# Optimization experiments

Hardware: AMD Instinct MI355X
Metric: run time of the kernel (lower is better)

Reference implementation:

```python
import jax, jax.numpy as jnp
import numpy as np

E = 65536            # total entities (flattened batch*history*slots)
ENTITY_SIZE = 256
NUM_SPECIES, NUM_ABILITIES, NUM_ITEMS, NUM_ACTIONS = 512, 128, 256, 512
# feature layout (column index in entity row)
SPECIES, ABILITY, ITEM = 0, 1, 2
SCALAR_FEATS = list(range(3, 16))   # level..fainted
SCALAR_MAX = [101, 2, 2, 32, 3, 8, 16, 2, 2, 2, 8, 4, 2]
BOOST_FEATS = list(range(16, 23))   # 7 boosts
BOOST_MAX = 13
VOL0, VOL8 = 23, 31                 # 9 uint16 volatile words
TC0, TC1 = 32, 33                   # 2 uint16 typechange words
MOVE0 = 34                          # 4 move-id tokens
NUM_FEATS = 38
HP_RATIO = 6
CONCAT_DIM = 512 + 128 + 256 + sum(SCALAR_MAX) + 7 * BOOST_MAX + 9 * 16 + 2 * 16 + 1  # = 1348

MAXES = np.ones(NUM_FEATS, dtype=np.int32)
MAXES[SPECIES], MAXES[ABILITY], MAXES[ITEM] = NUM_SPECIES, NUM_ABILITIES, NUM_ITEMS
for f, m in zip(SCALAR_FEATS, SCALAR_MAX):
    MAXES[f] = m
for f in BOOST_FEATS:
    MAXES[f] = BOOST_MAX
MAXES[VOL0:VOL8 + 1] = 65536
MAXES[TC0:TC1 + 1] = 65536
MAXES[MOVE0:MOVE0 + 4] = NUM_ACTIONS


def bits16(x):
    # x int32 [..., k] -> float bits [..., k*16]
    b = (x[..., None] >> jnp.arange(16, dtype=jnp.int32)) & 1
    return b.astype(jnp.float32).reshape(*x.shape[:-1], -1)


def setup_inputs() -> dict:
    key = jax.random.key(0)
    ks = jax.random.split(key, 12)
    u = jax.random.uniform(ks[0], (E, NUM_FEATS))
    entity = (u * jnp.asarray(MAXES, dtype=jnp.float32)).astype(jnp.int32)
    s = 0.02
    return {
        'entity': entity,
        'species_tbl': jax.random.normal(ks[1], (NUM_SPECIES, 512), jnp.float32) * s,
        'ability_tbl': jax.random.normal(ks[2], (NUM_ABILITIES, 128), jnp.float32) * s,
        'item_tbl': jax.random.normal(ks[3], (NUM_ITEMS, 256), jnp.float32) * s,
        'species_emb': jax.random.normal(ks[4], (NUM_SPECIES, ENTITY_SIZE), jnp.float32) * s,
        'ability_emb': jax.random.normal(ks[5], (NUM_ABILITIES, ENTITY_SIZE), jnp.float32) * s,
        'item_emb': jax.random.normal(ks[6], (NUM_ITEMS, ENTITY_SIZE), jnp.float32) * s,
        'actions_emb': jax.random.normal(ks[7], (NUM_ACTIONS, ENTITY_SIZE), jnp.float32) * s,
        'agg_w': jax.random.normal(ks[8], (CONCAT_DIM, ENTITY_SIZE), jnp.float32) * s,
        'agg_b': jnp.zeros((ENTITY_SIZE,), jnp.float32),
        'mlp_w': jax.random.normal(ks[9], (ENTITY_SIZE, ENTITY_SIZE), jnp.float32) * s,
        'mlp_b': jnp.zeros((ENTITY_SIZE,), jnp.float32),
    }


def reference(entity, species_tbl, ability_tbl, item_tbl, species_emb, ability_emb,
              item_emb, actions_emb, agg_w, agg_b, mlp_w, mlp_b):
    sp, ab, it = entity[:, SPECIES], entity[:, ABILITY], entity[:, ITEM]
    # pretrained one-hot / feature-table gathers
    enc = [species_tbl[sp], ability_tbl[ab], item_tbl[it]]
    # small scalar one-hots
    enc += [jax.nn.one_hot(entity[:, f], m, dtype=jnp.float32)
            for f, m in zip(SCALAR_FEATS, SCALAR_MAX)]
    # boost one-hots
    enc += [jax.nn.one_hot(entity[:, f], BOOST_MAX, dtype=jnp.float32) for f in BOOST_FEATS]
    # hex/binary encodings of volatile + typechange words
    enc.append(bits16(entity[:, VOL0:VOL8 + 1]))       # [E,144]
    enc.append(bits16(entity[:, TC0:TC1 + 1]))         # [E,32]
    # continuous feature (hp ratio)
    enc.append((entity[:, HP_RATIO].astype(jnp.float32) / 31.0)[:, None])
    concat = jnp.concatenate(enc, axis=-1)             # [E,1348]
    emb_sum = (species_emb[sp] + ability_emb[ab] + item_emb[it]
               + actions_emb[entity[:, MOVE0]] + actions_emb[entity[:, MOVE0 + 1]]
               + actions_emb[entity[:, MOVE0 + 2]] + actions_emb[entity[:, MOVE0 + 3]])
    x = concat @ agg_w + agg_b + emb_sum               # SumEmbeddings
    x = jax.nn.relu(x) @ mlp_w + mlp_b                 # MLP((entity_size,))
    mask = jnp.logical_and(sp != 0, sp != 1)           # not NULL / not PAD
    return jnp.where(mask[:, None], x, 0.0)
```

## Files before the change

kernel.cpp:

```cpp
#include <hip/hip_runtime.h>

#define NFEAT 38

typedef __attribute__((ext_vector_type(8))) short bf16x8;
typedef __attribute__((ext_vector_type(4))) float f32x4;
typedef __attribute__((ext_vector_type(2))) float f32x2;
typedef __attribute__((ext_vector_type(4))) unsigned int u32x4;

#define R_SP   0
#define R_AB   512
#define R_IT   640
#define R_T1   896
#define R_T2   1300
#define R_T3   1428
#define R_T4   1452
#define R_T5   1484
#define R_T6   1548
#define R_T7   1717
#define R_T8   1886
#define R_T9   2055
#define R_ACT  2068
#define NROWS  2580

#define B_FUSED  0
#define B_WMLP   224
#define B_WBITS  288
#define B_MERGED 336
#define B_IDXS   757
#define NB_PREP  821

__device__ __forceinline__ unsigned short f2bf(float f) {
    unsigned int u = __float_as_uint(f);
    u += 0x7fffu + ((u >> 16) & 1u);
    return (unsigned short)(u >> 16);
}

__global__ __launch_bounds__(1024) void k_prep(
    const float* __restrict__ sp_tbl, const float* __restrict__ ab_tbl,
    const float* __restrict__ it_tbl, const float* __restrict__ sp_emb,
    const float* __restrict__ ab_emb, const float* __restrict__ it_emb,
    const float* __restrict__ act_emb, const float* __restrict__ agg_w,
    const float* __restrict__ agg_b,  const float* __restrict__ mlp_w,
    const int* __restrict__ ent,
    unsigned short* __restrict__ tbl, unsigned short* __restrict__ wfrag,
    unsigned short* __restrict__ wbits, unsigned int* __restrict__ ridx)
{
    __shared__ float rowbuf[4 * 512];
    __shared__ float part[4][4][256];
    int blk = blockIdx.x, t = threadIdx.x, c = t & 255;
#define W(x) agg_w[(size_t)(x) * 256 + c]

    if (blk < B_WMLP) {
        int r0 = blk << 2;
        const float* src; const float* emb; int len, wbase; bool add_b;
        if (r0 < 512)      { src = sp_tbl + (size_t)r0 * 512;           emb = sp_emb + (size_t)r0 * 256;           len = 512; wbase = 0;   add_b = true;  }
        else if (r0 < 640) { int q = r0 - 512; src = ab_tbl + (size_t)q * 128; emb = ab_emb + (size_t)q * 256; len = 128; wbase = 512; add_b = false; }
        else               { int q = r0 - 640; src = it_tbl + (size_t)q * 256; emb = it_emb + (size_t)q * 256; len = 256; wbase = 640; add_b = false; }
        int tot = len << 2;
        for (int i = t; i < tot; i += 1024) rowbuf[i] = src[i];
        __syncthreads();
        int kq   = t >> 8;
        int len4 = len >> 2;
        int kbeg = kq * len4, kend = kbeg + len4;
        float a0 = 0.f, a1 = 0.f, a2 = 0.f, a3 = 0.f;
        #pragma unroll 4
        for (int k = kbeg; k < kend; ++k) {
            float w = W(wbase + k);
            a0 += rowbuf[k] * w;
            a1 += rowbuf[len + k] * w;
            a2 += rowbuf[2 * len + k] * w;
            a3 += rowbuf[3 * len + k] * w;
        }
        part[0][kq][c] = a0; part[1][kq][c] = a1;
        part[2][kq][c] = a2; part[3][kq][c] = a3;
        __syncthreads();
        int row = t >> 8;
        float s = part[row][0][c] + part[row][1][c] + part[row][2][c] + part[row][3][c]
                + emb[row * 256 + c] + (add_b ? agg_b[c] : 0.f);
        tbl[(size_t)(r0 + row) * 256 + c] = f2bf(s);
        return;
    }
    if (blk < B_WBITS) {
        int idx = ((blk - B_WMLP) << 10) + t;
        int j   = idx & 7;
        int fl  = (idx >> 3) & 63;
        int k0g = (idx >> 9) & 7;
        int nt  = idx >> 12;
        int k   = k0g * 32 + (fl >> 4) * 8 + j;
        int col = nt * 16 + (fl & 15);
        wfrag[idx] = f2bf(mlp_w[(size_t)k * 256 + col]);
        return;
    }
    if (blk < B_MERGED) {
        int idx = ((blk - B_WBITS) << 10) + t;
        int j   = idx & 7;
        int ln  = (idx >> 3) & 63;
        int r2  = idx >> 9;
        int kt  = r2 % 6;
        int nt  = r2 / 6;
        int k   = kt * 32 + ((ln >> 4) << 3) + j;
        int col = (nt << 4) + (ln & 15);
        float v = (k < 176) ? agg_w[(size_t)(1171 + k) * 256 + col] : 0.f;
        wbits[idx] = f2bf(v);
        return;
    }
    if (blk < B_IDXS) {
        int r = ((blk - B_MERGED) << 2) + (t >> 8);
        int row; float acc;
        if (r < 404)       { int f3 = r >> 2, f4 = (r >> 1) & 1, f5 = r & 1;
                             acc = W(896 + f3) + W(997 + f4) + W(999 + f5); row = R_T1 + r; }
        else if (r < 532)  { int i = r - 404; int f6 = i >> 2, f11 = (i >> 1) & 1, f12 = i & 1;
                             acc = W(1001 + f6) + (float)f6 * (1.f / 31.f) * W(1347)
                                 + W(1062 + f11) + W(1064 + f12); row = R_T2 + i; }
        else if (r < 556)  { int i = r - 532; acc = W(1033 + (i >> 3)) + W(1036 + (i & 7)); row = R_T3 + i; }
        else if (r < 588)  { int i = r - 556; acc = W(1044 + (i >> 1)) + W(1060 + (i & 1)); row = R_T4 + i; }
        else if (r < 652)  { int i = r - 588; acc = W(1066 + (i >> 3)) + W(1074 + ((i >> 1) & 3)) + W(1078 + (i & 1)); row = R_T5 + i; }
        else if (r < 821)  { int i = r - 652; acc = W(1080 + i / 13) + W(1093 + i % 13); row = R_T6 + i; }
        else if (r < 990)  { int i = r - 821; acc = W(1106 + i / 13) + W(1119 + i % 13); row = R_T7 + i; }
        else if (r < 1159) { int i = r - 990; acc = W(1132 + i / 13) + W(1145 + i % 13); row = R_T8 + i; }
        else if (r < 1172) { int i = r - 1159; acc = W(1158 + i); row = R_T9 + i; }
        else               { int i = r - 1172; acc = act_emb[(size_t)i * 256 + c]; row = R_ACT + i; }
        tbl[(size_t)row * 256 + c] = f2bf(acc);
        return;
    }
    {
        int e = ((blk - B_IDXS) << 10) + t;
        size_t bb = (size_t)e * (NFEAT * 4);
        const uint4* wp = reinterpret_cast<const uint4*>(
            reinterpret_cast<const char*>(ent) + (bb & ~(size_t)15));
        uint4 q0 = wp[0], q1 = wp[1], q2 = wp[2], q3 = wp[3], q4 = wp[4];
        uint4 q5 = wp[5], q6 = wp[6], q7 = wp[7], q8 = wp[8], q9 = wp[9];
        unsigned int v[40] = {q0.x,q0.y,q0.z,q0.w, q1.x,q1.y,q1.z,q1.w,
                              q2.x,q2.y,q2.z,q2.w, q3.x,q3.y,q3.z,q3.w,
                              q4.x,q4.y,q4.z,q4.w, q5.x,q5.y,q5.z,q5.w,
                              q6.x,q6.y,q6.z,q6.w, q7.x,q7.y,q7.z,q7.w,
                              q8.x,q8.y,q8.z,q8.w, q9.x,q9.y,q9.z,q9.w};
        int f[NFEAT];
        if (e & 1) {
            #pragma unroll
            for (int i = 0; i < NFEAT; ++i) f[i] = (int)v[i + 2];
        } else {
            #pragma unroll
            for (int i = 0; i < NFEAT; ++i) f[i] = (int)v[i];
        }
        int rw[16];
        rw[0]  = f[0];
        rw[1]  = R_AB + f[1];
        rw[2]  = R_IT + f[2];
        rw[3]  = R_T1 + f[3] * 4 + f[4] * 2 + f[5];
        rw[4]  = R_T2 + f[6] * 4 + f[11] * 2 + f[12];
        rw[5]  = R_T3 + f[7] * 8 + f[8];
        rw[6]  = R_T4 + f[9] * 2 + f[10];
        rw[7]  = R_T5 + f[13] * 8 + f[14] * 2 + f[15];
        rw[8]  = R_T6 + f[16] * 13 + f[17];
        rw[9]  = R_T7 + f[18] * 13 + f[19];
        rw[10] = R_T8 + f[20] * 13 + f[21];
        rw[11] = R_T9 + f[22];
        rw[12] = R_ACT + f[34];
        rw[13] = R_ACT + f[35];
        rw[14] = R_ACT + f[36];
        rw[15] = R_ACT + f[37];
        unsigned int p[16];
        #pragma unroll
        for (int i = 0; i < 8; ++i)
            p[i] = (unsigned int)rw[2 * i] | ((unsigned int)rw[2 * i + 1] << 16);
        #pragma unroll
        for (int i = 0; i < 5; ++i)
            p[8 + i] = (unsigned int)(f[23 + 2 * i] & 0xffff) | ((unsigned int)f[24 + 2 * i] << 16);
        p[13] = (unsigned int)(f[33] & 0xffff);
        p[14] = 0; p[15] = 0;
        uint4* dst = reinterpret_cast<uint4*>(ridx + (size_t)e * 16);
        dst[0] = make_uint4(p[0], p[1], p[2], p[3]);
        dst[1] = make_uint4(p[4], p[5], p[6], p[7]);
        dst[2] = make_uint4(p[8], p[9], p[10], p[11]);
        dst[3] = make_uint4(p[12], p[13], p[14], p[15]);
    }
#undef W
}

__global__ __launch_bounds__(512, 4) void k_fused_em(
    const unsigned int* __restrict__ ridx, const unsigned short* __restrict__ tbl,
    const unsigned short* __restrict__ wfrag, const unsigned short* __restrict__ wbits,
    const float* __restrict__ mlp_b, float* __restrict__ out)
{
    __shared__ float xacc[64 * 260];
    __shared__ unsigned int bitw[64 * 6];
    __shared__ unsigned char smask[64];
    int t    = threadIdx.x;
    int w    = t >> 6;
    int lane = t & 63;
    int half = lane >> 5;
    int cp   = lane & 31;
    int wu   = __builtin_amdgcn_readfirstlane(w);
    int eb   = blockIdx.x << 6;
    const char* tb = reinterpret_cast<const char*>(tbl);

    if (t < 384) {
        int e = t / 6, k = t - e * 6;
        bitw[t] = ridx[(size_t)(eb + e) * 16 + 8 + k];
    }
    if (t < 64) smask[t] = ((ridx[(size_t)(eb + t) * 16] & 0xffffu) < 2u) ? 1 : 0;

    {
        int cb = cp << 4;
        const unsigned int* rq0 = ridx + (size_t)(eb + (wu << 3)) * 16;
        uint4 v[8], vn[8];
        #pragma unroll
        for (int j = 0; j < 8; ++j) {
            unsigned int pj = rq0[j];
            unsigned int row = half ? (pj >> 16) : (pj & 0xffffu);
            v[j] = *reinterpret_cast<const uint4*>(tb + ((size_t)row << 9) + cb);
        }
        for (int i = 0; i < 8; ++i) {
            if (i < 7) {
                const unsigned int* rq = rq0 + ((i + 1) << 4);
                #pragma unroll
                for (int j = 0; j < 8; ++j) {
                    unsigned int pj = rq[j];
                    unsigned int row = half ? (pj >> 16) : (pj & 0xffffu);
                    vn[j] = *reinterpret_cast<const uint4*>(tb + ((size_t)row << 9) + cb);
                }
            }
            f32x2 aE0 = (f32x2){0.f, 0.f}, aO0 = (f32x2){0.f, 0.f};
            f32x2 aE1 = (f32x2){0.f, 0.f}, aO1 = (f32x2){0.f, 0.f};
            #pragma unroll
            for (int j = 0; j < 8; ++j) {
                aE0 += (f32x2){__uint_as_float(v[j].x << 16),         __uint_as_float(v[j].y << 16)};
                aO0 += (f32x2){__uint_as_float(v[j].x & 0xffff0000u), __uint_as_float(v[j].y & 0xffff0000u)};
                aE1 += (f32x2){__uint_as_float(v[j].z << 16),         __uint_as_float(v[j].w << 16)};
                aO1 += (f32x2){__uint_as_float(v[j].z & 0xffff0000u), __uint_as_float(v[j].w & 0xffff0000u)};
            }
            float s0 = aE0[0] + __shfl_xor(aE0[0], 32);
            float s1 = aO0[0] + __shfl_xor(aO0[0], 32);
            float s2 = aE0[1] + __shfl_xor(aE0[1], 32);
            float s3 = aO0[1] + __shfl_xor(aO0[1], 32);
            float s4 = aE1[0] + __shfl_xor(aE1[0], 32);
            float s5 = aO1[0] + __shfl_xor(aO1[0], 32);
            float s6 = aE1[1] + __shfl_xor(aE1[1], 32);
            float s7 = aO1[1] + __shfl_xor(aO1[1], 32);
            if (half == 0) {
                int el = (wu << 3) + i;
                float* dst = xacc + el * 260 + (cp << 3);
                *reinterpret_cast<float4*>(dst)     = make_float4(s0, s1, s2, s3);
                *reinterpret_cast<float4*>(dst + 4) = make_float4(s4, s5, s6, s7);
            }
            #pragma unroll
            for (int j = 0; j < 8; ++j) v[j] = vn[j];
        }
    }
    __syncthreads();

    int rc  = lane & 15;
    int kg  = lane >> 4;
    int nt0 = wu << 1;

    f32x4 D0[4], D1[4];
    #pragma unroll
    for (int mt = 0; mt < 4; ++mt) { D0[mt] = (f32x4){0.f,0.f,0.f,0.f}; D1[mt] = (f32x4){0.f,0.f,0.f,0.f}; }

    #pragma unroll
    for (int kt = 0; kt < 6; ++kt) {
        bf16x8 b0 = *reinterpret_cast<const bf16x8*>(wbits + (((size_t)(nt0 * 6 + kt)) << 9) + (lane << 3));
        bf16x8 b1 = *reinterpret_cast<const bf16x8*>(wbits + (((size_t)((nt0 + 1) * 6 + kt)) << 9) + (lane << 3));
        #pragma unroll
        for (int mt = 0; mt < 4; ++mt) {
            unsigned int wb = bitw[((mt << 4) + rc) * 6 + kt];
            unsigned int bs = wb >> (kg << 3);
            unsigned int e0 = ((bs & 1u)   ? 0x3F80u : 0u) | ((bs & 2u)   ? 0x3F800000u : 0u);
            unsigned int e1 = ((bs & 4u)   ? 0x3F80u : 0u) | ((bs & 8u)   ? 0x3F800000u : 0u);
            unsigned int e2 = ((bs & 16u)  ? 0x3F80u : 0u) | ((bs & 32u)  ? 0x3F800000u : 0u);
            unsigned int e3 = ((bs & 64u)  ? 0x3F80u : 0u) | ((bs & 128u) ? 0x3F800000u : 0u);
            bf16x8 afr = __builtin_bit_cast(bf16x8, (u32x4){e0, e1, e2, e3});
            D0[mt] = __builtin_amdgcn_mfma_f32_16x16x32_bf16(afr, b0, D0[mt], 0, 0, 0);
            D1[mt] = __builtin_amdgcn_mfma_f32_16x16x32_bf16(afr, b1, D1[mt], 0, 0, 0);
        }
    }

    unsigned short ov[32];
    #pragma unroll
    for (int mt = 0; mt < 4; ++mt) {
        #pragma unroll
        for (int j = 0; j < 4; ++j) {
            int row = (mt << 4) + (kg << 2) + j;
            int c0  = (wu << 5) + rc;
            float sA = xacc[row * 260 + c0]      + D0[mt][j];
            float sB = xacc[row * 260 + c0 + 16] + D1[mt][j];
            ov[(mt << 3) + j]     = f2bf(fmaxf(sA, 0.f));
            ov[(mt << 3) + 4 + j] = f2bf(fmaxf(sB, 0.f));
        }
    }
    __syncthreads();

    char* xb = reinterpret_cast<char*>(xacc);
    #pragma unroll
    for (int mt = 0; mt < 4; ++mt) {
        #pragma unroll
        for (int j = 0; j < 4; ++j) {
            int row = (mt << 4) + (kg << 2) + j;
            int colA = (wu << 5) + rc;
            int colB = colA + 16;
            int uA = (colA >> 3) ^ (row & 7);
            int uB = (colB >> 3) ^ (row & 7);
            *reinterpret_cast<unsigned short*>(xb + (row << 9) + (uA << 4) + ((colA & 7) << 1)) = ov[(mt << 3) + j];
            *reinterpret_cast<unsigned short*>(xb + (row << 9) + (uB << 4) + ((colB & 7) << 1)) = ov[(mt << 3) + 4 + j];
        }
    }
    __syncthreads();

    f32x4 acc0[4], acc1[4];
    #pragma unroll
    for (int mt = 0; mt < 4; ++mt) {
        acc0[mt] = (f32x4){0.f,0.f,0.f,0.f};
        acc1[mt] = (f32x4){0.f,0.f,0.f,0.f};
    }

    #pragma unroll
    for (int k0g = 0; k0g < 8; ++k0g) {
        bf16x8 b0 = *reinterpret_cast<const bf16x8*>(
            wfrag + (((size_t)(nt0 * 8 + k0g)) << 9) + (lane << 3));
        bf16x8 b1 = *reinterpret_cast<const bf16x8*>(
            wfrag + (((size_t)((nt0 + 1) * 8 + k0g)) << 9) + (lane << 3));
        int up = ((k0g << 2) + kg) ^ (rc & 7);
        #pragma unroll
        for (int mt = 0; mt < 4; ++mt) {
            int r = (mt << 4) + rc;
            bf16x8 a = *reinterpret_cast<const bf16x8*>(xb + (r << 9) + (up << 4));
            acc0[mt] = __builtin_amdgcn_mfma_f32_16x16x32_bf16(a, b0, acc0[mt], 0, 0, 0);
            acc1[mt] = __builtin_amdgcn_mfma_f32_16x16x32_bf16(a, b1, acc1[mt], 0, 0, 0);
        }
    }

    int c0 = wu << 5;
    float bias0 = mlp_b[c0 + rc];
    float bias1 = mlp_b[c0 + 16 + rc];
    #pragma unroll
    for (int mt = 0; mt < 4; ++mt) {
        unsigned int mw = *reinterpret_cast<const unsigned int*>(&smask[(mt << 4) + (kg << 2)]);
        #pragma unroll
        for (int j = 0; j < 4; ++j) {
            int row = eb + (mt << 4) + (kg << 2) + j;
            bool m = (mw >> (8 * j)) & 1u;
            out[(size_t)row * 256 + c0 + rc]      = m ? 0.f : (acc0[mt][j] + bias0);
            out[(size_t)row * 256 + c0 + 16 + rc] = m ? 0.f : (acc1[mt][j] + bias1);
        }
    }
}

extern "C" void kernel_launch(void* const* d_in, const int* in_sizes, int n_in,
                              void* d_out, int out_size, void* d_ws, size_t ws_size,
                              hipStream_t stream)
{
    const int*   ent     = (const int*)d_in[0];
    const float* sp_tbl  = (const float*)d_in[1];
    const float* ab_tbl  = (const float*)d_in[2];
    const float* it_tbl  = (const float*)d_in[3];
    const float* sp_emb  = (const float*)d_in[4];
    const float* ab_emb  = (const float*)d_in[5];
    const float* it_emb  = (const float*)d_in[6];
    const float* act_emb = (const float*)d_in[7];
    const float* agg_w   = (const float*)d_in[8];
    const float* agg_b   = (const float*)d_in[9];
    const float* mlp_w   = (const float*)d_in[10];
    const float* mlp_b   = (const float*)d_in[11];
    float* out = (float*)d_out;

    char* ws = (char*)d_ws;
    unsigned short* tbl   = (unsigned short*)(ws);
    unsigned short* wfrag = (unsigned short*)(ws + 1320960);
    unsigned short* wbits = (unsigned short*)(ws + 1452032);
    unsigned int*   ridx  = (unsigned int*)  (ws + 1550336);

    k_prep    <<<dim3(NB_PREP), dim3(1024), 0, stream>>>(sp_tbl, ab_tbl, it_tbl,
                                                         sp_emb, ab_emb, it_emb,
                                                         act_emb, agg_w, agg_b, mlp_w,
                                                         ent, tbl, wfrag, wbits, ridx);
    k_fused_em<<<dim3(1024),    dim3(512),  0, stream>>>(ridx, tbl, wfrag, wbits, mlp_b, out);
}
```

Baseline: 66.66 us.

## Store gathered embedding sums as bf16 in swizzled LDS and raise occupancy

The gathered embedding sum is now stored directly as bf16 in the swizzled LDS layout, halving the shared buffer (about 66KB down to 32KB). The bits-MFMA result is added in place, which removes one __syncthreads and the separate fp32-to-bf16 copy. The gather software prefetch (double-buffered vn registers) is dropped and launch bounds go to 8 blocks per CU to cut register pressure and raise occupancy. This rounds the embedding sum to bf16 before the add and ReLU, and latency hiding now relies on occupancy instead of explicit prefetch.

After: 69.66 us. 1.04x slower.

```diff
diff --git a/kernel.cpp b/kernel.cpp
--- a/kernel.cpp
+++ b/kernel.cpp
@@ -178,12 +178,12 @@
 #undef W
 }
 
-__global__ __launch_bounds__(512, 4) void k_fused_em(
+__global__ __launch_bounds__(512, 8) void k_fused_em(
     const unsigned int* __restrict__ ridx, const unsigned short* __restrict__ tbl,
     const unsigned short* __restrict__ wfrag, const unsigned short* __restrict__ wbits,
     const float* __restrict__ mlp_b, float* __restrict__ out)
 {
-    __shared__ float xacc[64 * 260];
+    __shared__ unsigned short xw[64 * 256];
     __shared__ unsigned int bitw[64 * 6];
     __shared__ unsigned char smask[64];
     int t    = threadIdx.x;
@@ -194,6 +194,7 @@
     int wu   = __builtin_amdgcn_readfirstlane(w);
     int eb   = blockIdx.x << 6;
     const char* tb = reinterpret_cast<const char*>(tbl);
+    char* xb = reinterpret_cast<char*>(xw);
 
     if (t < 384) {
         int e = t / 6, k = t - e * 6;
@@ -203,23 +204,15 @@
 
     {
         int cb = cp << 4;
-        const unsigned int* rq0 = ridx + (size_t)(eb + (wu << 3)) * 16;
-        uint4 v[8], vn[8];
-        #pragma unroll
-        for (int j = 0; j < 8; ++j) {
-            unsigned int pj = rq0[j];
-            unsigned int row = half ? (pj >> 16) : (pj & 0xffffu);
-            v[j] = *reinterpret_cast<const uint4*>(tb + ((size_t)row << 9) + cb);
-        }
         for (int i = 0; i < 8; ++i) {
-            if (i < 7) {
-                const unsigned int* rq = rq0 + ((i + 1) << 4);
-                #pragma unroll
-                for (int j = 0; j < 8; ++j) {
-                    unsigned int pj = rq[j];
-                    unsigned int row = half ? (pj >> 16) : (pj & 0xffffu);
-                    vn[j] = *reinterpret_cast<const uint4*>(tb + ((size_t)row << 9) + cb);
-                }
+            int el = (wu << 3) + i;
+            const unsigned int* rq = ridx + (size_t)(eb + el) * 16;
+            uint4 v[8];
+            #pragma unroll
+            for (int j = 0; j < 8; ++j) {
+                unsigned int pj = rq[j];
+                unsigned int row = half ? (pj >> 16) : (pj & 0xffffu);
+                v[j] = *reinterpret_cast<const uint4*>(tb + ((size_t)row << 9) + cb);
             }
             f32x2 aE0 = (f32x2){0.f, 0.f}, aO0 = (f32x2){0.f, 0.f};
             f32x2 aE1 = (f32x2){0.f, 0.f}, aO1 = (f32x2){0.f, 0.f};
@@ -239,13 +232,13 @@
             float s6 = aE1[1] + __shfl_xor(aE1[1], 32);
             float s7 = aO1[1] + __shfl_xor(aO1[1], 32);
             if (half == 0) {
-                int el = (wu << 3) + i;
-                float* dst = xacc + el * 260 + (cp << 3);
-                *reinterpret_cast<float4*>(dst)     = make_float4(s0, s1, s2, s3);
-                *reinterpret_cast<float4*>(dst + 4) = make_float4(s4, s5, s6, s7);
+                unsigned int o0 = (unsigned)f2bf(s0) | ((unsigned)f2bf(s1) << 16);
+                unsigned int o1 = (unsigned)f2bf(s2) | ((unsigned)f2bf(s3) << 16);
+                unsigned int o2 = (unsigned)f2bf(s4) | ((unsigned)f2bf(s5) << 16);
+                unsigned int o3 = (unsigned)f2bf(s6) | ((unsigned)f2bf(s7) << 16);
+                int up = cp ^ (el & 7);
+                *reinterpret_cast<uint4*>(xb + (el << 9) + (up << 4)) = make_uint4(o0, o1, o2, o3);
             }
-            #pragma unroll
-            for (int j = 0; j < 8; ++j) v[j] = vn[j];
         }
     }
     __syncthreads();
@@ -253,6 +246,7 @@
     int rc  = lane & 15;
     int kg  = lane >> 4;
     int nt0 = wu << 1;
+    int c0  = wu << 5;
 
     f32x4 D0[4], D1[4];
     #pragma unroll
@@ -276,33 +270,23 @@
         }
     }
 
-    unsigned short ov[32];
     #pragma unroll
     for (int mt = 0; mt < 4; ++mt) {
         #pragma unroll
         for (int j = 0; j < 4; ++j) {
-            int row = (mt << 4) + (kg << 2) + j;
-            int c0  = (wu << 5) + rc;
-            float sA = xacc[row * 260 + c0]      + D0[mt][j];
-            float sB = xacc[row * 260 + c0 + 16] + D1[mt][j];
-            ov[(mt << 3) + j]     = f2bf(fmaxf(sA, 0.f));
-            ov[(mt << 3) + 4 + j] = f2bf(fmaxf(sB, 0.f));
-        }
-    }
-    __syncthreads();
-
-    char* xb = reinterpret_cast<char*>(xacc);
-    #pragma unroll
-    for (int mt = 0; mt < 4; ++mt) {
-        #pragma unroll
-        for (int j = 0; j < 4; ++j) {
-            int row = (mt << 4) + (kg << 2) + j;
-            int colA = (wu << 5) + rc;
+            int row  = (mt << 4) + (kg << 2) + j;
+            int colA = c0 + rc;
             int colB = colA + 16;
             int uA = (colA >> 3) ^ (row & 7);
             int uB = (colB >> 3) ^ (row & 7);
-            *reinterpret_cast<unsigned short*>(xb + (row << 9) + (uA << 4) + ((colA & 7) << 1)) = ov[(mt << 3) + j];
-            *reinterpret_cast<unsigned short*>(xb + (row << 9) + (uB << 4) + ((colB & 7) << 1)) = ov[(mt << 3) + 4 + j];
+            unsigned short* pA = reinterpret_cast<unsigned short*>(
+                xb + (row << 9) + (uA << 4) + ((colA & 7) << 1));
+            unsigned short* pB = reinterpret_cast<unsigned short*>(
+                xb + (row << 9) + (uB << 4) + ((colB & 7) << 1));
+            float xA = __uint_as_float((unsigned int)(*pA) << 16) + D0[mt][j];
+            float xB = __uint_as_float((unsigned int)(*pB) << 16) + D1[mt][j];
+            *pA = f2bf(fmaxf(xA, 0.f));
+            *pB = f2bf(fmaxf(xB, 0.f));
         }
     }
     __syncthreads();
@@ -330,7 +314,6 @@
         }
     }
 
-    int c0 = wu << 5;
     float bias0 = mlp_b[c0 + rc];
     float bias1 = mlp_b[c0 + 16 + rc];
     #pragma unroll
```
